# Kernel tuning notes

Measured on AMD Instinct MI355X. Metric: run time of the kernel, lower is better.

## Reference

```python
import jax, jax.numpy as jnp
import numpy as np

N = 50000       # nodes
E = 800000      # edges (before self loops)
DIN = 128       # input feature width
H = 4           # heads
C = 64          # hidden width per head
NCLS = 2        # num classes
NEG_SLOPE = 0.2 # PyG GATConv default negative_slope


def setup_inputs() -> dict:
    key = jax.random.key(0)
    ks = jax.random.split(key, 16)
    x = jax.random.normal(ks[0], (N, DIN), dtype=jnp.float32)
    edge_index = jax.random.randint(ks[1], (2, E), 0, N, dtype=jnp.int64)
    s = 0.05
    # layer 0: DIN -> H*C
    W0 = jax.random.normal(ks[2], (DIN, H * C), dtype=jnp.float32) * s
    a_src0 = jax.random.normal(ks[3], (H, C), dtype=jnp.float32) * s
    a_dst0 = jax.random.normal(ks[4], (H, C), dtype=jnp.float32) * s
    b0 = jnp.zeros((H * C,), dtype=jnp.float32)
    # layer 1: H*C -> H*C
    W1 = jax.random.normal(ks[5], (H * C, H * C), dtype=jnp.float32) * s
    a_src1 = jax.random.normal(ks[6], (H, C), dtype=jnp.float32) * s
    a_dst1 = jax.random.normal(ks[7], (H, C), dtype=jnp.float32) * s
    b1 = jnp.zeros((H * C,), dtype=jnp.float32)
    # layer 2: H*C -> NCLS, single head
    W2 = jax.random.normal(ks[8], (H * C, NCLS), dtype=jnp.float32) * s
    a_src2 = jax.random.normal(ks[9], (1, NCLS), dtype=jnp.float32) * s
    a_dst2 = jax.random.normal(ks[10], (1, NCLS), dtype=jnp.float32) * s
    b2 = jnp.zeros((NCLS,), dtype=jnp.float32)
    return {"x": x, "edge_index": edge_index,
            "W0": W0, "a_src0": a_src0, "a_dst0": a_dst0, "b0": b0,
            "W1": W1, "a_src1": a_src1, "a_dst1": a_dst1, "b1": b1,
            "W2": W2, "a_src2": a_src2, "a_dst2": a_dst2, "b2": b2}


def gat_conv(x, ei, W, a_src, a_dst, b, heads, out_c):
    """PyG-style GATConv (add_self_loops already applied to ei, concat=True)."""
    n = x.shape[0]
    h = (x @ W).reshape(n, heads, out_c)              # [N, H, C]
    src, dst = ei[0], ei[1]
    asrc = (h * a_src).sum(-1)                         # [N, H]
    adst = (h * a_dst).sum(-1)                         # [N, H]
    alpha = jax.nn.leaky_relu(asrc[src] + adst[dst], NEG_SLOPE)  # [E', H]
    # segment softmax over incoming edges of each dst node
    amax = jax.ops.segment_max(alpha, dst, num_segments=n)        # [N, H]
    e = jnp.exp(alpha - amax[dst])
    denom = jax.ops.segment_sum(e, dst, num_segments=n)
    coef = e / denom[dst]                              # [E', H]
    msg = h[src] * coef[:, :, None]                    # [E', H, C]
    out = jax.ops.segment_sum(msg, dst, num_segments=n)           # [N, H, C]
    return out.reshape(n, heads * out_c) + b


def reference(x, edge_index, W0, a_src0, a_dst0, b0,
              W1, a_src1, a_dst1, b1, W2, a_src2, a_dst2, b2):
    # Inference mode: dropout(p=0.5, training=False) is identity.
    loops = jnp.arange(N, dtype=edge_index.dtype)
    ei = jnp.concatenate([edge_index, jnp.stack([loops, loops])], axis=1)
    h = jnp.tanh(gat_conv(x, ei, W0, a_src0, a_dst0, b0, H, C))
    h = jnp.tanh(gat_conv(h, ei, W1, a_src1, a_dst1, b1, H, C))
    h = gat_conv(h, ei, W2, a_src2, a_dst2, b2, 1, NCLS)
    return jax.nn.softmax(h, axis=1), h
```

## Files before the change

### kernel.cpp

```cpp
#include <hip/hip_runtime.h>
#include <hip/hip_bf16.h>

#define NEG 0.2f

typedef float f32x4 __attribute__((ext_vector_type(4)));
typedef short bf16x8 __attribute__((ext_vector_type(8)));

struct __align__(8) us4 { unsigned short v[4]; };

__device__ __forceinline__ float b2f(unsigned short u){
  union { unsigned int i; float f; } x; x.i = ((unsigned int)u) << 16; return x.f;
}
__device__ __forceinline__ unsigned short f2b(float f){
  __hip_bfloat16 h = __float2bfloat16(f);
  return *reinterpret_cast<unsigned short*>(&h);
}

__global__ __launch_bounds__(256) void k_setup(
    const float* __restrict__ W0, unsigned short* __restrict__ Wp0,
    const float* __restrict__ W1, unsigned short* __restrict__ Wp1,
    const int* __restrict__ ei, int* __restrict__ meta,
    int* __restrict__ deg, int N, int npack){
  const int bid = blockIdx.x;
  if (bid < npack){
    int t = bid*256 + threadIdx.x;
    const int T0 = 16*4*64;
    const int T1 = 16*8*64;
    const float* W; unsigned short* Wp;
    if (t < T0){ W = W0; Wp = Wp0; }
    else if (t < T0 + T1){ W = W1; Wp = Wp1; t -= T0; }
    else return;
    int lane = t & 63;
    int nb = (t >> 6) & 15;
    int kb = (t >> 6) >> 4;
    int kbase = kb*32 + ((lane>>4)<<3);
    int col = nb*16 + (lane&15);
    #pragma unroll
    for (int j=0;j<8;j++) Wp[(size_t)t*8 + j] = f2b(W[(size_t)(kbase+j)*256 + col]);
  } else {
    int i = (bid - npack)*256 + threadIdx.x;
    if (i < N) deg[i] = 0;
    if (i == 0){
      int o = 0;
      #pragma unroll
      for (int j=1;j<128;j+=2) o |= ei[j];
      meta[0] = (o==0) ? 1 : 0;
    }
  }
}

template<int K, int CVT>
__device__ __forceinline__ void gemm_body(int bid, const void* __restrict__ Xv,
    const unsigned short* __restrict__ Wp,
    const float* __restrict__ aS, const float* __restrict__ aD,
    unsigned short* __restrict__ Hout,
    float* __restrict__ asrc, float* __restrict__ adst, int N){
  constexpr int KB = K/32;
  __shared__ short sB[2][16*64*8];
  const int lane = threadIdx.x & 63;
  const int wave = threadIdx.x >> 6;
  const int rowbase = bid*64 + wave*16;
  const int l15 = lane & 15, lhi = lane >> 4;
  const int arow = rowbase + l15;

  bf16x8 aF[KB];
  if (CVT){
    const float* X = (const float*)Xv;
    #pragma unroll
    for (int kb=0; kb<KB; kb++){
      bf16x8 a = {};
      if (arow < N){
        f32x4 v0 = *(const f32x4*)(X + (size_t)arow*K + kb*32 + lhi*8);
        f32x4 v1 = *(const f32x4*)(X + (size_t)arow*K + kb*32 + lhi*8 + 4);
        #pragma unroll
        for (int j=0;j<4;j++){ a[j] = (short)f2b(v0[j]); a[j+4] = (short)f2b(v1[j]); }
      }
      aF[kb] = a;
    }
  } else {
    const unsigned short* X = (const unsigned short*)Xv;
    #pragma unroll
    for (int kb=0; kb<KB; kb++){
      bf16x8 a = {};
      if (arow < N) a = *(const bf16x8*)(X + (size_t)arow*K + kb*32 + lhi*8);
      aF[kb] = a;
    }
  }

  auto stage = [&](int buf, int kb){
    #pragma unroll
    for (int q=0;q<4;q++){
      int nb = wave*4 + q;
      const unsigned short* gsrc = Wp + ((size_t)((kb*16 + nb)*64) + lane)*8;
      __builtin_amdgcn_global_load_lds(
          (const __attribute__((address_space(1))) void*)gsrc,
          (__attribute__((address_space(3))) void*)&sB[buf][(size_t)nb*64*8],
          16, 0, 0);
    }
  };

  f32x4 acc[16] = {};
  stage(0, 0);
  __syncthreads();
  #pragma unroll
  for (int kb=0; kb<KB; kb++){
    const int cur = kb & 1;
    if (kb+1 < KB) stage(cur^1, kb+1);
    #pragma unroll
    for (int nb=0; nb<16; nb++){
      bf16x8 b = *(const bf16x8*)(&sB[cur][((size_t)nb*64 + lane)*8]);
      acc[nb] = __builtin_amdgcn_mfma_f32_16x16x32_bf16(aF[kb], b, acc[nb], 0, 0, 0);
    }
    __syncthreads();
  }

  const int r0 = rowbase + lhi*4;

  float sp[4][4] = {}; float dp[4][4] = {};
  #pragma unroll
  for (int h=0; h<4; h++){
    #pragma unroll
    for (int q=0; q<4; q++){
      const int nb = h*4 + q;
      float ws = aS[h*64 + q*16 + l15];
      float wd = aD[h*64 + q*16 + l15];
      #pragma unroll
      for (int r=0;r<4;r++){ sp[r][h] += acc[nb][r]*ws; dp[r][h] += acc[nb][r]*wd; }
    }
  }
  #pragma unroll
  for (int m=1;m<16;m<<=1){
    #pragma unroll
    for (int r=0;r<4;r++){
      #pragma unroll
      for (int h=0;h<4;h++){
        sp[r][h] += __shfl_xor(sp[r][h], m);
        dp[r][h] += __shfl_xor(dp[r][h], m);
      }
    }
  }
  if (l15 < 4){
    const int h = l15;
    #pragma unroll
    for (int r=0;r<4;r++){
      int row = r0 + r;
      if (row < N){ asrc[row*4+h] = sp[r][h]; adst[row*4+h] = dp[r][h]; }
    }
  }
  #pragma unroll
  for (int nb=0;nb<16;nb++){
    #pragma unroll
    for (int r=0;r<4;r++){
      int row = r0 + r;
      if (row < N) Hout[(size_t)row*256 + nb*16 + l15] = f2b(acc[nb][r]);
    }
  }
}

__global__ __launch_bounds__(256) void k_g128deg(
    const float* __restrict__ x, const unsigned short* __restrict__ Wp0,
    const float* __restrict__ aS, const float* __restrict__ aD,
    unsigned short* __restrict__ hb,
    float* __restrict__ asrc, float* __restrict__ adst, int N,
    const int* __restrict__ ei, const int* __restrict__ meta,
    int* __restrict__ deg, int E, int EP, int ngemm){
  const int bid = blockIdx.x;
  if (bid < ngemm){
    gemm_body<128,1>(bid, x, Wp0, aS, aD, hb, asrc, adst, N);
  } else {
    int e = (bid - ngemm)*256 + threadIdx.x;
    if (e >= EP) return;
    int d;
    if (e < E) d = meta[0] ? ei[2*(size_t)(E+e)] : ei[E+e];
    else       d = e - E;
    if ((unsigned)d >= (unsigned)N) return;
    atomicAdd(deg + d, 1);
  }
}

__global__ __launch_bounds__(256) void k_gemm256(const unsigned short* __restrict__ X,
    const unsigned short* __restrict__ Wp,
    const float* __restrict__ aS, const float* __restrict__ aD,
    unsigned short* __restrict__ Hout,
    float* __restrict__ asrc, float* __restrict__ adst, int N){
  gemm_body<256,0>(blockIdx.x, X, Wp, aS, aD, Hout, asrc, adst, N);
}


__global__ void k_scan1(const int* __restrict__ deg, int* __restrict__ tmp,
                        int* __restrict__ bsum, int N){
  __shared__ int s[256];
  int t = threadIdx.x;
  int i = blockIdx.x*256 + t;
  int v = (i < N) ? deg[i] : 0;
  s[t] = v;
  __syncthreads();
  for (int off=1; off<256; off<<=1){
    int x = (t>=off) ? s[t-off] : 0;
    __syncthreads();
    s[t] += x;
    __syncthreads();
  }
  if (i < N) tmp[i] = s[t] - v;
  if (t == 255) bsum[blockIdx.x] = s[255];
}

__global__ void k_scan2(const int* __restrict__ bsum, int* __restrict__ bsumx,
                        int* __restrict__ meta, int n){
  __shared__ int s[256];
  int t = threadIdx.x;
  int v = (t < n) ? bsum[t] : 0;
  s[t] = v;
  __syncthreads();
  for (int off=1; off<256; off<<=1){
    int x = (t>=off) ? s[t-off] : 0;
    __syncthreads();
    s[t] += x;
    __syncthreads();
  }
  bsumx[t] = s[t] - v;
  if (t == 255) meta[1] = s[255];
}

__global__ void k_scan3(const int* __restrict__ tmp, const int* __restrict__ bsumx,
                        const int* __restrict__ meta,
                        int* __restrict__ rp, int* __restrict__ cur, int N){
  int i = blockIdx.x*256 + threadIdx.x;
  if (i < N){ int v = tmp[i] + bsumx[i>>8]; rp[i] = v; cur[i] = v; }
  if (i == 0) rp[N] = meta[1];
}

__global__ void k_fill(const int* __restrict__ ei, const int* __restrict__ meta,
                       int* __restrict__ cur, int* __restrict__ csr, int E, int EP, int N){
  int e = blockIdx.x*blockDim.x + threadIdx.x;
  if (e >= EP) return;
  int s, d;
  if (e < E){
    if (meta[0]){ s = ei[2*(size_t)e]; d = ei[2*(size_t)(E+e)]; }
    else        { s = ei[e];           d = ei[E+e]; }
  } else { s = d = e - E; }
  if ((unsigned)d >= (unsigned)N) return;
  int pos = atomicAdd(cur + d, 1);
  csr[pos] = s;
}

__global__ __launch_bounds__(256) void k_agg(const unsigned short* __restrict__ Hb,
    const float* __restrict__ asrc, const float* __restrict__ adst,
    const int* __restrict__ rp, const int* __restrict__ csr,
    const float* __restrict__ bias, unsigned short* __restrict__ Xout, int N){
  const int lane = threadIdx.x & 63;
  const int dst = blockIdx.x*4 + (threadIdx.x >> 6);
  if (dst >= N) return;
  const int head = lane >> 4;
  const int c0 = lane*4;
  const float ad = adst[dst*4 + head];
  const int s0 = rp[dst], s1 = rp[dst+1];
  float a0=0.f,a1=0.f,a2=0.f,a3=0.f,den=0.f;
  int e = s0;
  for (; e+8 <= s1; e += 8){
    int i0 = csr[e+0], i1 = csr[e+1], i2 = csr[e+2], i3 = csr[e+3];
    int i4 = csr[e+4], i5 = csr[e+5], i6 = csr[e+6], i7 = csr[e+7];
    float x0 = asrc[(size_t)i0*4 + head];
    float x1 = asrc[(size_t)i1*4 + head];
    float x2 = asrc[(size_t)i2*4 + head];
    float x3 = asrc[(size_t)i3*4 + head];
    float x4 = asrc[(size_t)i4*4 + head];
    float x5 = asrc[(size_t)i5*4 + head];
    float x6 = asrc[(size_t)i6*4 + head];
    float x7 = asrc[(size_t)i7*4 + head];
    us4 h0 = *(const us4*)(Hb + (size_t)i0*256 + c0);
    us4 h1 = *(const us4*)(Hb + (size_t)i1*256 + c0);
    us4 h2 = *(const us4*)(Hb + (size_t)i2*256 + c0);
    us4 h3 = *(const us4*)(Hb + (size_t)i3*256 + c0);
    us4 h4 = *(const us4*)(Hb + (size_t)i4*256 + c0);
    us4 h5 = *(const us4*)(Hb + (size_t)i5*256 + c0);
    us4 h6 = *(const us4*)(Hb + (size_t)i6*256 + c0);
    us4 h7 = *(const us4*)(Hb + (size_t)i7*256 + c0);
    x0 += ad; x0 = x0 > 0.f ? x0 : NEG*x0; float e0 = __expf(x0);
    x1 += ad; x1 = x1 > 0.f ? x1 : NEG*x1; float e1 = __expf(x1);
    x2 += ad; x2 = x2 > 0.f ? x2 : NEG*x2; float e2 = __expf(x2);
    x3 += ad; x3 = x3 > 0.f ? x3 : NEG*x3; float e3 = __expf(x3);
    x4 += ad; x4 = x4 > 0.f ? x4 : NEG*x4; float e4 = __expf(x4);
    x5 += ad; x5 = x5 > 0.f ? x5 : NEG*x5; float e5 = __expf(x5);
    x6 += ad; x6 = x6 > 0.f ? x6 : NEG*x6; float e6 = __expf(x6);
    x7 += ad; x7 = x7 > 0.f ? x7 : NEG*x7; float e7 = __expf(x7);
    den += ((e0+e1)+(e2+e3)) + ((e4+e5)+(e6+e7));
    a0 += e0*b2f(h0.v[0]) + e1*b2f(h1.v[0]) + e2*b2f(h2.v[0]) + e3*b2f(h3.v[0])
        + e4*b2f(h4.v[0]) + e5*b2f(h5.v[0]) + e6*b2f(h6.v[0]) + e7*b2f(h7.v[0]);
    a1 += e0*b2f(h0.v[1]) + e1*b2f(h1.v[1]) + e2*b2f(h2.v[1]) + e3*b2f(h3.v[1])
        + e4*b2f(h4.v[1]) + e5*b2f(h5.v[1]) + e6*b2f(h6.v[1]) + e7*b2f(h7.v[1]);
    a2 += e0*b2f(h0.v[2]) + e1*b2f(h1.v[2]) + e2*b2f(h2.v[2]) + e3*b2f(h3.v[2])
        + e4*b2f(h4.v[2]) + e5*b2f(h5.v[2]) + e6*b2f(h6.v[2]) + e7*b2f(h7.v[2]);
    a3 += e0*b2f(h0.v[3]) + e1*b2f(h1.v[3]) + e2*b2f(h2.v[3]) + e3*b2f(h3.v[3])
        + e4*b2f(h4.v[3]) + e5*b2f(h5.v[3]) + e6*b2f(h6.v[3]) + e7*b2f(h7.v[3]);
  }
  for (; e+4 <= s1; e += 4){
    int i0 = csr[e+0], i1 = csr[e+1], i2 = csr[e+2], i3 = csr[e+3];
    float x0 = asrc[(size_t)i0*4 + head];
    float x1 = asrc[(size_t)i1*4 + head];
    float x2 = asrc[(size_t)i2*4 + head];
    float x3 = asrc[(size_t)i3*4 + head];
    us4 h0 = *(const us4*)(Hb + (size_t)i0*256 + c0);
    us4 h1 = *(const us4*)(Hb + (size_t)i1*256 + c0);
    us4 h2 = *(const us4*)(Hb + (size_t)i2*256 + c0);
    us4 h3 = *(const us4*)(Hb + (size_t)i3*256 + c0);
    x0 += ad; x0 = x0 > 0.f ? x0 : NEG*x0; float e0 = __expf(x0);
    x1 += ad; x1 = x1 > 0.f ? x1 : NEG*x1; float e1 = __expf(x1);
    x2 += ad; x2 = x2 > 0.f ? x2 : NEG*x2; float e2 = __expf(x2);
    x3 += ad; x3 = x3 > 0.f ? x3 : NEG*x3; float e3 = __expf(x3);
    den += (e0 + e1) + (e2 + e3);
    a0 += e0*b2f(h0.v[0]) + e1*b2f(h1.v[0]) + e2*b2f(h2.v[0]) + e3*b2f(h3.v[0]);
    a1 += e0*b2f(h0.v[1]) + e1*b2f(h1.v[1]) + e2*b2f(h2.v[1]) + e3*b2f(h3.v[1]);
    a2 += e0*b2f(h0.v[2]) + e1*b2f(h1.v[2]) + e2*b2f(h2.v[2]) + e3*b2f(h3.v[2]);
    a3 += e0*b2f(h0.v[3]) + e1*b2f(h1.v[3]) + e2*b2f(h2.v[3]) + e3*b2f(h3.v[3]);
  }
  for (; e < s1; e++){
    int src = csr[e];
    float al = asrc[(size_t)src*4 + head] + ad;
    al = al > 0.f ? al : NEG*al;
    float ee = __expf(al);
    den += ee;
    us4 hv = *(const us4*)(Hb + (size_t)src*256 + c0);
    a0 += ee * b2f(hv.v[0]);
    a1 += ee * b2f(hv.v[1]);
    a2 += ee * b2f(hv.v[2]);
    a3 += ee * b2f(hv.v[3]);
  }
  float rd = 1.0f/den;
  us4 o;
  o.v[0] = f2b(tanhf(a0*rd + bias[c0+0]));
  o.v[1] = f2b(tanhf(a1*rd + bias[c0+1]));
  o.v[2] = f2b(tanhf(a2*rd + bias[c0+2]));
  o.v[3] = f2b(tanhf(a3*rd + bias[c0+3]));
  *(us4*)(Xout + (size_t)dst*256 + c0) = o;
}

__global__ __launch_bounds__(256) void k_gemm2(const unsigned short* __restrict__ X,
    const float* __restrict__ W2, const float* __restrict__ as2, const float* __restrict__ ad2,
    float* __restrict__ H2, float* __restrict__ asrc2, float* __restrict__ adst2, int N){
  __shared__ float sW[512];
  const int t = threadIdx.x;
  sW[t] = W2[t]; sW[t+256] = W2[t+256];
  __syncthreads();
  const int row = blockIdx.x*16 + (t>>4);
  const int sub = t & 15;
  float a0=0.f, a1=0.f;
  if (row < N){
    const unsigned short* xp = X + (size_t)row*256 + sub*16;
    #pragma unroll
    for (int jj=0;jj<4;jj++){
      us4 hv = *(const us4*)(xp + jj*4);
      #pragma unroll
      for (int j=0;j<4;j++){
        float f = b2f(hv.v[j]);
        int k = sub*16 + jj*4 + j;
        a0 += f * sW[k*2+0];
        a1 += f * sW[k*2+1];
      }
    }
  }
  #pragma unroll
  for (int m=1;m<16;m<<=1){ a0 += __shfl_xor(a0,m); a1 += __shfl_xor(a1,m); }
  if (sub==0 && row<N){
    H2[row*2+0]=a0; H2[row*2+1]=a1;
    asrc2[row] = a0*as2[0] + a1*as2[1];
    adst2[row] = a0*ad2[0] + a1*ad2[1];
  }
}

__global__ __launch_bounds__(256) void k_agg2(const float* __restrict__ H2,
    const float* __restrict__ asrc2, const float* __restrict__ adst2,
    const int* __restrict__ rp, const int* __restrict__ csr, const float* __restrict__ bb,
    float* __restrict__ out, int N){
  const int sub = threadIdx.x & 15;
  const int dst = blockIdx.x*16 + (threadIdx.x >> 4);
  if (dst >= N) return;
  const float ad = adst2[dst];
  const int s0 = rp[dst], s1 = rp[dst+1];
  float n0=0.f, n1=0.f, den=0.f;
  for (int e=s0+sub; e<s1; e+=16){
    int src = csr[e];
    float al = asrc2[src] + ad;
    al = al>0.f ? al : NEG*al;
    float ee = __expf(al);
    den += ee;
    n0 += ee * H2[src*2+0];
    n1 += ee * H2[src*2+1];
  }
  #pragma unroll
  for (int m=1;m<16;m<<=1){
    n0 += __shfl_xor(n0,m); n1 += __shfl_xor(n1,m); den += __shfl_xor(den,m);
  }
  if (sub==0){
    float o0 = n0/den + bb[0];
    float o1 = n1/den + bb[1];
    float mx = fmaxf(o0,o1);
    float e0 = __expf(o0-mx), e1 = __expf(o1-mx);
    float is = 1.0f/(e0+e1);
    out[(size_t)dst*2+0] = e0*is;
    out[(size_t)dst*2+1] = e1*is;
    out[(size_t)2*N + dst*2+0] = o0;
    out[(size_t)2*N + dst*2+1] = o1;
  }
}

extern "C" void kernel_launch(void* const* d_in, const int* in_sizes, int n_in,
                              void* d_out, int out_size, void* d_ws, size_t ws_size,
                              hipStream_t stream){
  const float* x  = (const float*)d_in[0];
  const int*   ei = (const int*)d_in[1];
  const float* W0 = (const float*)d_in[2];
  const float* as0= (const float*)d_in[3];
  const float* ad0= (const float*)d_in[4];
  const float* b0 = (const float*)d_in[5];
  const float* W1 = (const float*)d_in[6];
  const float* as1= (const float*)d_in[7];
  const float* ad1= (const float*)d_in[8];
  const float* b1 = (const float*)d_in[9];
  const float* W2 = (const float*)d_in[10];
  const float* as2= (const float*)d_in[11];
  const float* ad2= (const float*)d_in[12];
  const float* b2 = (const float*)d_in[13];

  const int N  = in_sizes[0] / 128;
  const int E  = in_sizes[1] / 2;
  const int EP = E + N;
  float* outp = (float*)d_out;

  char* w = (char*)d_ws;
  size_t off = 0;
  auto alloc = [&](size_t bytes)->char*{
    char* p = w + off; off = (off + bytes + 255) & ~(size_t)255; return p;
  };
  unsigned short* hb  = (unsigned short*)alloc((size_t)N*256*2);
  unsigned short* xa  = (unsigned short*)alloc((size_t)N*256*2);
  float* asrc  = (float*)alloc((size_t)N*4*4);
  float* adst  = (float*)alloc((size_t)N*4*4);
  float* asrc2 = (float*)alloc((size_t)N*4);
  float* adst2 = (float*)alloc((size_t)N*4);
  float* H2    = (float*)alloc((size_t)N*2*4);
  unsigned short* Wp0 = (unsigned short*)alloc((size_t)128*256*2);
  unsigned short* Wp1 = (unsigned short*)alloc((size_t)256*256*2);
  int* deg   = (int*)alloc((size_t)N*4);
  int* rp    = (int*)alloc((size_t)(N+1)*4);
  int* cur   = (int*)alloc((size_t)N*4);
  int* tmp   = (int*)alloc((size_t)N*4);
  int* bsum  = (int*)alloc(256*4);
  int* bsumx = (int*)alloc(256*4);
  int* meta  = (int*)alloc(8*4);
  int* csr   = (int*)alloc((size_t)EP*4);
  (void)ws_size; (void)n_in; (void)out_size;

  const int npack = (16*4*64 + 16*8*64) / 256;
  const int ninit = (N + 255)/256;
  k_setup<<<npack + ninit, 256, 0, stream>>>(W0, Wp0, W1, Wp1, ei, meta, deg, N, npack);

  const int ngemm = (N + 63)/64;
  const int ndeg  = (EP + 255)/256;
  k_g128deg<<<ngemm + ndeg, 256, 0, stream>>>(x, Wp0, as0, ad0, hb, asrc, adst, N,
                                              ei, meta, deg, E, EP, ngemm);

  const int nb1 = (N + 255)/256;
  k_scan1 <<<nb1, 256, 0, stream>>>(deg, tmp, bsum, N);
  k_scan2 <<<1, 256, 0, stream>>>(bsum, bsumx, meta, nb1);
  k_scan3 <<<nb1, 256, 0, stream>>>(tmp, bsumx, meta, rp, cur, N);
  k_fill  <<<ndeg, 256, 0, stream>>>(ei, meta, cur, csr, E, EP, N);

  k_agg   <<<(N + 3)/4, 256, 0, stream>>>(hb, asrc, adst, rp, csr, b0, xa, N);
  k_gemm256<<<ngemm, 256, 0, stream>>>(xa, Wp1, as1, ad1, hb, asrc, adst, N);
  k_agg   <<<(N + 3)/4, 256, 0, stream>>>(hb, asrc, adst, rp, csr, b1, xa, N);
  k_gemm2 <<<(N + 15)/16, 256, 0, stream>>>(xa, W2, as2, ad2, H2, asrc2, adst2, N);
  k_agg2  <<<(N + 15)/16, 256, 0, stream>>>(H2, asrc2, adst2, rp, csr, b2, outp, N);
}
```

Baseline: 289.4 us.

## Fuse final layer projection into second aggregation and batch degree counting

The second aggregation kernel now computes the layer-2 projection (256->2) and its attention logits in its epilogue, using a wave-wide shuffle reduction. This removes the k_gemm2 launch and the bf16 write and re-read of the full 256-wide hidden activations. The degree-count part of the fused GEMM/degree kernel now has each thread handle four edges, cutting the number of extra blocks. The cost is a 64-lane shuffle reduction per destination node, plus slightly different rounding since the projection now uses fp32 activations instead of bf16.

```diff
diff --git a/kernel.cpp b/kernel.cpp
--- a/kernel.cpp
+++ b/kernel.cpp
@@ -168,13 +168,17 @@
   if (bid < ngemm){
     gemm_body<128,1>(bid, x, Wp0, aS, aD, hb, asrc, adst, N);
   } else {
-    int e = (bid - ngemm)*256 + threadIdx.x;
-    if (e >= EP) return;
-    int d;
-    if (e < E) d = meta[0] ? ei[2*(size_t)(E+e)] : ei[E+e];
-    else       d = e - E;
-    if ((unsigned)d >= (unsigned)N) return;
-    atomicAdd(deg + d, 1);
+    int base = ((bid - ngemm)*256 + threadIdx.x)*4;
+    const int m0 = meta[0];
+    #pragma unroll
+    for (int j=0;j<4;j++){
+      int e = base + j;
+      if (e >= EP) break;
+      int d;
+      if (e < E) d = m0 ? ei[2*(size_t)(E+e)] : ei[E+e];
+      else       d = e - E;
+      if ((unsigned)d < (unsigned)N) atomicAdd(deg + d, 1);
+    }
   }
 }
 
@@ -244,10 +248,14 @@
   csr[pos] = s;
 }
 
+template<int FUSE2>
 __global__ __launch_bounds__(256) void k_agg(const unsigned short* __restrict__ Hb,
     const float* __restrict__ asrc, const float* __restrict__ adst,
     const int* __restrict__ rp, const int* __restrict__ csr,
-    const float* __restrict__ bias, unsigned short* __restrict__ Xout, int N){
+    const float* __restrict__ bias, unsigned short* __restrict__ Xout, int N,
+    const float* __restrict__ W2, const float* __restrict__ as2,
+    const float* __restrict__ ad2,
+    float* __restrict__ H2, float* __restrict__ asrc2, float* __restrict__ adst2){
   const int lane = threadIdx.x & 63;
   const int dst = blockIdx.x*4 + (threadIdx.x >> 6);
   if (dst >= N) return;
@@ -327,44 +335,28 @@
     a3 += ee * b2f(hv.v[3]);
   }
   float rd = 1.0f/den;
-  us4 o;
-  o.v[0] = f2b(tanhf(a0*rd + bias[c0+0]));
-  o.v[1] = f2b(tanhf(a1*rd + bias[c0+1]));
-  o.v[2] = f2b(tanhf(a2*rd + bias[c0+2]));
-  o.v[3] = f2b(tanhf(a3*rd + bias[c0+3]));
-  *(us4*)(Xout + (size_t)dst*256 + c0) = o;
-}
-
-__global__ __launch_bounds__(256) void k_gemm2(const unsigned short* __restrict__ X,
-    const float* __restrict__ W2, const float* __restrict__ as2, const float* __restrict__ ad2,
-    float* __restrict__ H2, float* __restrict__ asrc2, float* __restrict__ adst2, int N){
-  __shared__ float sW[512];
-  const int t = threadIdx.x;
-  sW[t] = W2[t]; sW[t+256] = W2[t+256];
-  __syncthreads();
-  const int row = blockIdx.x*16 + (t>>4);
-  const int sub = t & 15;
-  float a0=0.f, a1=0.f;
-  if (row < N){
-    const unsigned short* xp = X + (size_t)row*256 + sub*16;
-    #pragma unroll
-    for (int jj=0;jj<4;jj++){
-      us4 hv = *(const us4*)(xp + jj*4);
-      #pragma unroll
-      for (int j=0;j<4;j++){
-        float f = b2f(hv.v[j]);
-        int k = sub*16 + jj*4 + j;
-        a0 += f * sW[k*2+0];
-        a1 += f * sW[k*2+1];
-      }
-    }
-  }
-  #pragma unroll
-  for (int m=1;m<16;m<<=1){ a0 += __shfl_xor(a0,m); a1 += __shfl_xor(a1,m); }
-  if (sub==0 && row<N){
-    H2[row*2+0]=a0; H2[row*2+1]=a1;
-    asrc2[row] = a0*as2[0] + a1*as2[1];
-    adst2[row] = a0*ad2[0] + a1*ad2[1];
+  f32x4 bv = *(const f32x4*)(bias + c0);
+  float o0 = tanhf(a0*rd + bv[0]);
+  float o1 = tanhf(a1*rd + bv[1]);
+  float o2 = tanhf(a2*rd + bv[2]);
+  float o3 = tanhf(a3*rd + bv[3]);
+  if (FUSE2){
+    f32x4 w01 = *(const f32x4*)(W2 + c0*2);
+    f32x4 w23 = *(const f32x4*)(W2 + c0*2 + 4);
+    float p0 = o0*w01[0] + o1*w01[2] + o2*w23[0] + o3*w23[2];
+    float p1 = o0*w01[1] + o1*w01[3] + o2*w23[1] + o3*w23[3];
+    #pragma unroll
+    for (int m=1;m<64;m<<=1){ p0 += __shfl_xor(p0,m); p1 += __shfl_xor(p1,m); }
+    if (lane == 0){
+      H2[(size_t)dst*2+0] = p0;
+      H2[(size_t)dst*2+1] = p1;
+      asrc2[dst] = p0*as2[0] + p1*as2[1];
+      adst2[dst] = p0*ad2[0] + p1*ad2[1];
+    }
+  } else {
+    us4 o;
+    o.v[0] = f2b(o0); o.v[1] = f2b(o1); o.v[2] = f2b(o2); o.v[3] = f2b(o3);
+    *(us4*)(Xout + (size_t)dst*256 + c0) = o;
   }
 }
 
@@ -456,7 +448,7 @@
   k_setup<<<npack + ninit, 256, 0, stream>>>(W0, Wp0, W1, Wp1, ei, meta, deg, N, npack);
 
   const int ngemm = (N + 63)/64;
-  const int ndeg  = (EP + 255)/256;
+  const int ndeg  = (EP + 1023)/1024;
   k_g128deg<<<ngemm + ndeg, 256, 0, stream>>>(x, Wp0, as0, ad0, hb, asrc, adst, N,
                                               ei, meta, deg, E, EP, ngemm);
 
@@ -464,11 +456,12 @@
   k_scan1 <<<nb1, 256, 0, stream>>>(deg, tmp, bsum, N);
   k_scan2 <<<1, 256, 0, stream>>>(bsum, bsumx, meta, nb1);
   k_scan3 <<<nb1, 256, 0, stream>>>(tmp, bsumx, meta, rp, cur, N);
-  k_fill  <<<ndeg, 256, 0, stream>>>(ei, meta, cur, csr, E, EP, N);
-
-  k_agg   <<<(N + 3)/4, 256, 0, stream>>>(hb, asrc, adst, rp, csr, b0, xa, N);
+  k_fill  <<<(EP + 255)/256, 256, 0, stream>>>(ei, meta, cur, csr, E, EP, N);
+
+  k_agg<0><<<(N + 3)/4, 256, 0, stream>>>(hb, asrc, adst, rp, csr, b0, xa, N,
+                                          nullptr, nullptr, nullptr, nullptr, nullptr, nullptr);
   k_gemm256<<<ngemm, 256, 0, stream>>>(xa, Wp1, as1, ad1, hb, asrc, adst, N);
-  k_agg   <<<(N + 3)/4, 256, 0, stream>>>(hb, asrc, adst, rp, csr, b1, xa, N);
-  k_gemm2 <<<(N + 15)/16, 256, 0, stream>>>(xa, W2, as2, ad2, H2, asrc2, adst2, N);
+  k_agg<1><<<(N + 3)/4, 256, 0, stream>>>(hb, asrc, adst, rp, csr, b1, nullptr, N,
+                                          W2, as2, ad2, H2, asrc2, adst2);
   k_agg2  <<<(N + 15)/16, 256, 0, stream>>>(H2, asrc2, adst2, rp, csr, b2, outp, N);
 }
```

Result: faster. 278.1 us, median of 2 (-3.9%).
